# Optimization experiments

Measured on AMD Instinct MI355X. Metric: run time of the kernel, lower is better.

Reference implementation:

```python
import jax, jax.numpy as jnp
import numpy as np

B, T, DIM, H, DH = 4, 2048, 1024, 16, 64
NEG = -1.0e9


def setup_inputs() -> dict:
    key = jax.random.key(0)
    ks = jax.random.split(key, 12)
    inner = H * DH
    s_in = 1.0 / np.sqrt(DIM)
    s_out = 1.0 / np.sqrt(inner)
    q = jax.random.normal(ks[0], (B, T, DIM), jnp.float32)
    k = jax.random.normal(ks[1], (B, T, DIM), jnp.float32)
    v = jax.random.normal(ks[2], (B, T, DIM), jnp.float32)
    # nn.Linear weights stored as [out, in]; we keep [in, out] for x @ W
    W_q = jax.random.uniform(ks[3], (DIM, inner), jnp.float32, -s_in, s_in)
    b_q = jax.random.uniform(ks[4], (inner,), jnp.float32, -s_in, s_in)
    W_k = jax.random.uniform(ks[5], (DIM, inner), jnp.float32, -s_in, s_in)
    b_k = jax.random.uniform(ks[6], (inner,), jnp.float32, -s_in, s_in)
    W_v = jax.random.uniform(ks[7], (DIM, inner), jnp.float32, -s_in, s_in)
    b_v = jax.random.uniform(ks[8], (inner,), jnp.float32, -s_in, s_in)
    W_o = jax.random.uniform(ks[9], (inner, DIM), jnp.float32, -s_out, s_out)
    b_o = jax.random.uniform(ks[10], (DIM,), jnp.float32, -s_out, s_out)
    # causal mask: True = masked (strict upper triangle), broadcastable [1,1,T,T]
    causal_mask = jnp.triu(jnp.ones((T, T), bool), k=1)[None, None]
    # context mask: True = keep; random padding pattern with col 0 always valid
    context_mask = jax.random.bernoulli(ks[11], 0.9, (B, T)).at[:, 0].set(True)
    return {"q": q, "k": k, "v": v,
            "W_q": W_q, "b_q": b_q, "W_k": W_k, "b_k": b_k,
            "W_v": W_v, "b_v": b_v, "W_o": W_o, "b_o": b_o,
            "causal_mask": causal_mask, "context_mask": context_mask}


def reference(q, k, v, W_q, b_q, W_k, b_k, W_v, b_v, W_o, b_o,
              causal_mask, context_mask):
    scale = DH ** -0.5
    split = lambda x: x.reshape(x.shape[0], x.shape[1], H, DH).transpose(0, 2, 1, 3)
    qh = split(q @ W_q + b_q)  # [b,h,t,d]
    kh = split(k @ W_k + b_k)
    vh = split(v @ W_v + b_v)
    scores = jnp.einsum('bhid,bhjd->bhij', qh * scale, kh)
    scores = jnp.where(context_mask[:, None, None, :], scores, NEG)
    scores = jnp.where(causal_mask, NEG, scores)
    probs = jax.nn.softmax(scores, axis=-1)
    out = jnp.einsum('bhij,bhjd->bhid', probs, vh)
    out = out.transpose(0, 2, 1, 3).reshape(B, T, H * DH)
    return out @ W_o + b_o
```

## Files before the change

kernel.cpp:

```cpp
#include <hip/hip_runtime.h>
#include <hip/hip_bf16.h>
#include <cstdint>
#include <cstddef>

#define DEV static __device__ __forceinline__

typedef __attribute__((ext_vector_type(8))) short short8;
typedef __attribute__((ext_vector_type(4))) float floatx4;

#define BB 4
#define TT 2048
#define DIMM 1024
#define HH 16
#define DHH 64
#define MM (BB*TT)
#define QBLK 128
#define NQT (TT/QBLK)
#define M0F 12.0f

DEV unsigned short f2bu(float f) {
    unsigned int u = __float_as_uint(f);
    unsigned int r = (u + 0x7fffu + ((u >> 16) & 1u)) >> 16;
    return (unsigned short)r;
}

DEV unsigned long long pack4(float a, float b, float c, float d) {
    return (unsigned long long)f2bu(a) | ((unsigned long long)f2bu(b) << 16) |
           ((unsigned long long)f2bu(c) << 32) | ((unsigned long long)f2bu(d) << 48);
}

DEV unsigned int pk2(float lo, float hi) {
    __hip_bfloat162 h = __float22bfloat162_rn(make_float2(lo, hi));
    unsigned int r;
    __builtin_memcpy(&r, &h, 4);
    return r;
}

DEV unsigned long long pk4(float a, float b, float c, float d) {
    return (unsigned long long)pk2(a, b) | ((unsigned long long)pk2(c, d) << 32);
}

DEV void gload16(const void* g, void* l) {
    __builtin_amdgcn_global_load_lds(
        (const __attribute__((address_space(1))) unsigned int*)g,
        (__attribute__((address_space(3))) unsigned int*)l, 16, 0, 0);
}

#define MFMA16(a, b, c) __builtin_amdgcn_mfma_f32_16x16x32_bf16((a), (b), (c), 0, 0, 0)

__global__ __launch_bounds__(256) void ctx_bias(const unsigned char* __restrict__ raw,
                                                float* __restrict__ out) {
    __shared__ int nz1, nz23;
    if (threadIdx.x == 0) { nz1 = 0; nz23 = 0; }
    __syncthreads();
    int a1 = 0, a23 = 0;
    for (int i = threadIdx.x; i < BB * TT; i += 256) {
        unsigned char vb = raw[i];
        int m = i & 3;
        if (vb) { if (m == 1) a1 = 1; else if (m >= 2) a23 = 1; }
    }
    if (a1) atomicOr(&nz1, 1);
    if (a23) atomicOr(&nz23, 1);
    __syncthreads();
    const int mode = nz1 ? 2 : (nz23 ? 1 : 0);
    for (int i = threadIdx.x; i < BB * TT; i += 256) {
        bool keep;
        if (mode == 2)      keep = raw[i] != 0;
        else if (mode == 0) keep = raw[(size_t)4 * i] != 0;
        else                keep = (raw[(size_t)4 * i + 2] | raw[(size_t)4 * i + 3]) != 0;
        out[i] = keep ? -M0F : -3.0e38f;
    }
}

__global__ __launch_bounds__(256) void wtrans(const float* __restrict__ W0, const float* __restrict__ W1,
                                              const float* __restrict__ W2, const float* __restrict__ W3,
                                              unsigned short* __restrict__ out) {
    const float* W = blockIdx.y == 0 ? W0 : blockIdx.y == 1 ? W1 : blockIdx.y == 2 ? W2 : W3;
    unsigned short* O = out + (size_t)blockIdx.y * DIMM * DIMM;
    const int tx = blockIdx.x & 15, ty = blockIdx.x >> 4;
    __shared__ float s[64][65];
    const int tid = threadIdx.x;
#pragma unroll
    for (int j = 0; j < 4; ++j) {
        int c = tid + 256 * j;
        int r = c >> 4, c4 = c & 15;
        float4 vv = *reinterpret_cast<const float4*>(&W[(size_t)(ty * 64 + r) * DIMM + tx * 64 + c4 * 4]);
        s[r][c4 * 4 + 0] = vv.x; s[r][c4 * 4 + 1] = vv.y;
        s[r][c4 * 4 + 2] = vv.z; s[r][c4 * 4 + 3] = vv.w;
    }
    __syncthreads();
#pragma unroll
    for (int j = 0; j < 4; ++j) {
        int c = tid + 256 * j;
        int n = c >> 4, k4 = c & 15;
        unsigned long long pk = pack4(s[k4 * 4 + 0][n], s[k4 * 4 + 1][n], s[k4 * 4 + 2][n], s[k4 * 4 + 3][n]);
        *reinterpret_cast<unsigned long long*>(&O[(size_t)(tx * 64 + n) * DIMM + ty * 64 + k4 * 4]) = pk;
    }
}

__global__ __launch_bounds__(256) void proj3(const float* __restrict__ qin, const float* __restrict__ kin,
                                             const float* __restrict__ vin, const unsigned short* __restrict__ Wt,
                                             const float* __restrict__ bq, const float* __restrict__ bk,
                                             const float* __restrict__ bv,
                                             unsigned short* __restrict__ Qp, unsigned short* __restrict__ Kp,
                                             unsigned short* __restrict__ Vtp, float scale_q) {
    const int z = blockIdx.z;
    const float* Af = z == 0 ? qin : z == 1 ? kin : vin;
    const unsigned short* Bt = Wt + (size_t)z * DIMM * DIMM;
    const float* bias = z == 0 ? bq : z == 1 ? bk : bv;
    const float scale = z == 0 ? scale_q : 1.f;

    __shared__ unsigned short As[128 * 32];
    __shared__ unsigned short Bs[128 * 32];
    const int tid = threadIdx.x, lane = tid & 63, g = lane >> 4, lq = lane & 15;
    const int wid = tid >> 6;
    const int mbase = blockIdx.x * 128, nbase = blockIdx.y * 128;
    const int wm = (wid >> 1) * 64, wn = (wid & 1) * 64;
    floatx4 acc[4][4];
#pragma unroll
    for (int i = 0; i < 4; ++i)
#pragma unroll
        for (int j = 0; j < 4; ++j) acc[i][j] = (floatx4){0.f, 0.f, 0.f, 0.f};

    for (int k0 = 0; k0 < DIMM; k0 += 32) {
#pragma unroll
        for (int j = 0; j < 2; ++j) {
            int c = j * 256 + tid;
            int row = c >> 2, kc = c & 3;
            gload16(&Bt[(size_t)(nbase + row) * DIMM + k0 + kc * 8], &Bs[c * 8]);
        }
#pragma unroll
        for (int j = 0; j < 4; ++j) {
            int c = tid + 256 * j;
            int row = c >> 3, kc = c & 7;
            float4 v = *reinterpret_cast<const float4*>(&Af[(size_t)(mbase + row) * DIMM + k0 + kc * 4]);
            *reinterpret_cast<unsigned long long*>(&As[row * 32 + kc * 4]) = pk4(v.x, v.y, v.z, v.w);
        }
        __syncthreads();
        short8 af[4], bfr[4];
#pragma unroll
        for (int i = 0; i < 4; ++i) {
            af[i]  = *reinterpret_cast<const short8*>(&As[(wm + i * 16 + lq) * 32 + g * 8]);
            bfr[i] = *reinterpret_cast<const short8*>(&Bs[(wn + i * 16 + lq) * 32 + g * 8]);
        }
#pragma unroll
        for (int i = 0; i < 4; ++i)
#pragma unroll
            for (int j = 0; j < 4; ++j)
                acc[i][j] = MFMA16(af[i], bfr[j], acc[i][j]);
        __syncthreads();
    }

#pragma unroll
    for (int i = 0; i < 4; ++i) {
#pragma unroll
        for (int j = 0; j < 4; ++j) {
            const int col = nbase + wn + j * 16 + lq;
            const float bvv = bias[col];
            const int row0 = mbase + wm + i * 16 + g * 4;
            if (z < 2) {
                unsigned short* C = z == 0 ? Qp : Kp;
#pragma unroll
                for (int r = 0; r < 4; ++r)
                    C[(size_t)(row0 + r) * DIMM + col] = f2bu((acc[i][j][r] + bvv) * scale);
            } else {
                const int b = row0 >> 11, t0 = row0 & (TT - 1);
                const int h = col >> 6, d = col & 63;
                unsigned long long pk = pk4(acc[i][j][0] + bvv, acc[i][j][1] + bvv,
                                            acc[i][j][2] + bvv, acc[i][j][3] + bvv);
                *reinterpret_cast<unsigned long long*>(
                    &Vtp[((size_t)(b * HH + h) * DHH + d) * TT + t0]) = pk;
            }
        }
    }
}

__global__ __launch_bounds__(256) void gemm_out(const unsigned short* __restrict__ Ab,
                                                const unsigned short* __restrict__ Bt,
                                                const float* __restrict__ bias,
                                                float* __restrict__ C) {
    __shared__ unsigned short As[128 * 32];
    __shared__ unsigned short Bs[128 * 32];
    const int tid = threadIdx.x, lane = tid & 63, g = lane >> 4, lq = lane & 15;
    const int wid = tid >> 6;
    const int mbase = blockIdx.x * 128, nbase = blockIdx.y * 128;
    const int wm = (wid >> 1) * 64, wn = (wid & 1) * 64;
    floatx4 acc[4][4];
#pragma unroll
    for (int i = 0; i < 4; ++i)
#pragma unroll
        for (int j = 0; j < 4; ++j) acc[i][j] = (floatx4){0.f, 0.f, 0.f, 0.f};

    for (int k0 = 0; k0 < DIMM; k0 += 32) {
#pragma unroll
        for (int j = 0; j < 2; ++j) {
            int c = j * 256 + tid;
            int row = c >> 2, kc = c & 3;
            gload16(&Bt[(size_t)(nbase + row) * DIMM + k0 + kc * 8], &Bs[c * 8]);
            gload16(&Ab[(size_t)(mbase + row) * DIMM + k0 + kc * 8], &As[c * 8]);
        }
        __syncthreads();
        short8 af[4], bfr[4];
#pragma unroll
        for (int i = 0; i < 4; ++i) {
            af[i]  = *reinterpret_cast<const short8*>(&As[(wm + i * 16 + lq) * 32 + g * 8]);
            bfr[i] = *reinterpret_cast<const short8*>(&Bs[(wn + i * 16 + lq) * 32 + g * 8]);
        }
#pragma unroll
        for (int i = 0; i < 4; ++i)
#pragma unroll
            for (int j = 0; j < 4; ++j)
                acc[i][j] = MFMA16(af[i], bfr[j], acc[i][j]);
        __syncthreads();
    }

#pragma unroll
    for (int i = 0; i < 4; ++i) {
#pragma unroll
        for (int j = 0; j < 4; ++j) {
            const int col = nbase + wn + j * 16 + lq;
            const float bv = bias[col];
            const int row0 = mbase + wm + i * 16 + g * 4;
#pragma unroll
            for (int r = 0; r < 4; ++r)
                C[(size_t)(row0 + r) * DIMM + col] = acc[i][j][r] + bv;
        }
    }
}

__global__ __launch_bounds__(512, 4) void attn128(const unsigned short* __restrict__ Q,
                                                  const unsigned short* __restrict__ Km,
                                                  const unsigned short* __restrict__ Vt,
                                                  const float* __restrict__ ctxb,
                                                  unsigned short* __restrict__ O) {
    const int pair = blockIdx.x & 7, h = (blockIdx.x >> 3) & 15, b = blockIdx.x >> 7;
    const int tid = threadIdx.x, lane = tid & 63, g = lane >> 4, lq = lane & 15, wid = tid >> 6;

    __shared__ unsigned short Qs[QBLK * 64];
    __shared__ unsigned short Ks[2][64 * 64];
    __shared__ unsigned short Vs[2][64 * 64];
    __shared__ unsigned short Ps[8][16 * 72];

    const float* cbias = ctxb + b * TT;
    const unsigned short* Vbase = Vt + (size_t)(b * HH + h) * DHH * TT;
    const int srow = tid >> 3, sdc = tid & 7;
    const int soff = (srow * 128 + sdc * 16) ^ ((srow & 7) << 4);

    for (int part = 0; part < 2; ++part) {
        const int qt = (part == 0) ? pair : (NQT - 1 - pair);
        const int qbase = qt * QBLK;
        const size_t rowQ = (size_t)(b * TT + qbase);
        const int nkv = 2 * qt + 2;

        __syncthreads();
#pragma unroll
        for (int j = 0; j < 2; ++j) {
            int ci = j * 512 + tid;
            int row = ci >> 3, dc = ci & 7;
            *reinterpret_cast<float4*>((char*)Qs + ((row * 128 + dc * 16) ^ ((row & 7) << 4))) =
                *reinterpret_cast<const float4*>(&Q[(rowQ + row) * DIMM + h * DHH + dc * 8]);
        }
        {
            float4 k0v = *reinterpret_cast<const float4*>(&Km[(size_t)(b * TT + srow) * DIMM + h * DHH + sdc * 8]);
            float4 v0v = *reinterpret_cast<const float4*>(&Vbase[(size_t)srow * TT + sdc * 8]);
            *reinterpret_cast<float4*>((char*)Ks[0] + soff) = k0v;
            *reinterpret_cast<float4*>((char*)Vs[0] + soff) = v0v;
        }
        __syncthreads();

        short8 qf0, qf1;
        {
            const int r = wid * 16 + lq;
            const int sw = (r & 7) << 4;
            qf0 = *reinterpret_cast<const short8*>((char*)Qs + ((r * 128 + g * 16) ^ sw));
            qf1 = *reinterpret_cast<const short8*>((char*)Qs + ((r * 128 + 64 + g * 16) ^ sw));
        }

        floatx4 oacc[4];
#pragma unroll
        for (int f = 0; f < 4; ++f) oacc[f] = (floatx4){0.f, 0.f, 0.f, 0.f};
        float l_run = 0.f;
        const int qwave_min = qbase + wid * 16;
        const int qg = qwave_min + lq;

        for (int kt = 0; kt < nkv; ++kt) {
            const int cur = kt & 1;
            const int kvb = kt * 64;
            const bool pf = (kt + 1 < nkv);
            float4 kreg, vreg;
            if (pf) {
                const int kvn = kvb + 64;
                kreg = *reinterpret_cast<const float4*>(&Km[(size_t)(b * TT + kvn + srow) * DIMM + h * DHH + sdc * 8]);
                vreg = *reinterpret_cast<const float4*>(&Vbase[(size_t)srow * TT + kvn + sdc * 8]);
            }
            if (kvb <= qwave_min + 15) {
                const bool needC = (kvb + 63 > qwave_min);
                float p[4][4];
                __builtin_amdgcn_s_setprio(1);
#pragma unroll
                for (int f = 0; f < 4; ++f) {
                    const int r = f * 16 + lq;
                    const int sw = (r & 7) << 4;
                    short8 kf0 = *reinterpret_cast<const short8*>((char*)Ks[cur] + ((r * 128 + g * 16) ^ sw));
                    short8 kf1 = *reinterpret_cast<const short8*>((char*)Ks[cur] + ((r * 128 + 64 + g * 16) ^ sw));
                    const float4 bias = *reinterpret_cast<const float4*>(&cbias[kvb + f * 16 + g * 4]);
                    floatx4 t = (floatx4){bias.x, bias.y, bias.z, bias.w};
                    t = MFMA16(kf0, qf0, t);
                    t = MFMA16(kf1, qf1, t);
#pragma unroll
                    for (int r2 = 0; r2 < 4; ++r2) {
                        float sv = t[r2];
                        if (needC) {
                            const int kv = kvb + f * 16 + g * 4 + r2;
                            if (kv > qg) sv = -3.0e38f;
                        }
                        p[f][r2] = exp2f(sv);
                    }
                }
                __builtin_amdgcn_s_setprio(0);
                float rs = 0.f;
#pragma unroll
                for (int f = 0; f < 4; ++f)
#pragma unroll
                    for (int r2 = 0; r2 < 4; ++r2) rs += p[f][r2];
                rs += __shfl_xor(rs, 16, 64);
                rs += __shfl_xor(rs, 32, 64);
                l_run += rs;
#pragma unroll
                for (int f = 0; f < 4; ++f)
                    *reinterpret_cast<unsigned long long*>(&Ps[wid][lq * 72 + f * 16 + g * 4]) =
                        pk4(p[f][0], p[f][1], p[f][2], p[f][3]);
                __builtin_amdgcn_s_setprio(1);
#pragma unroll
                for (int f = 0; f < 4; ++f) {
                    const int r = f * 16 + lq;
                    const int sw = (r & 7) << 4;
#pragma unroll
                    for (int kk = 0; kk < 2; ++kk) {
                        short8 av = *reinterpret_cast<const short8*>((char*)Vs[cur] + ((r * 128 + kk * 64 + g * 16) ^ sw));
                        short8 bv = *reinterpret_cast<const short8*>(&Ps[wid][lq * 72 + kk * 32 + g * 8]);
                        oacc[f] = MFMA16(av, bv, oacc[f]);
                    }
                }
                __builtin_amdgcn_s_setprio(0);
            }
            if (pf) {
                *reinterpret_cast<float4*>((char*)Ks[cur ^ 1] + soff) = kreg;
                *reinterpret_cast<float4*>((char*)Vs[cur ^ 1] + soff) = vreg;
            }
            __syncthreads();
        }

        const float inv = 1.f / l_run;
#pragma unroll
        for (int f = 0; f < 4; ++f) {
            unsigned long long pk = pk4(oacc[f][0] * inv, oacc[f][1] * inv,
                                        oacc[f][2] * inv, oacc[f][3] * inv);
            *reinterpret_cast<unsigned long long*>(
                &O[(rowQ + wid * 16 + lq) * DIMM + h * DHH + f * 16 + g * 4]) = pk;
        }
    }
}

extern "C" void kernel_launch(void* const* d_in, const int* in_sizes, int n_in,
                              void* d_out, int out_size, void* d_ws, size_t ws_size,
                              hipStream_t stream) {
    const float* q  = (const float*)d_in[0];
    const float* k  = (const float*)d_in[1];
    const float* v  = (const float*)d_in[2];
    const float* Wq = (const float*)d_in[3];
    const float* bq = (const float*)d_in[4];
    const float* Wk = (const float*)d_in[5];
    const float* bk = (const float*)d_in[6];
    const float* Wv = (const float*)d_in[7];
    const float* bv = (const float*)d_in[8];
    const float* Wo = (const float*)d_in[9];
    const float* bo = (const float*)d_in[10];
    const unsigned char* cmask = (const unsigned char*)d_in[12];

    unsigned short* Qp  = (unsigned short*)d_ws;
    unsigned short* Kp  = Qp + (size_t)MM * DIMM;
    unsigned short* Vtp = Kp + (size_t)MM * DIMM;
    unsigned short* AO  = Vtp + (size_t)MM * DIMM;
    unsigned short* Wt  = AO + (size_t)MM * DIMM;
    float* ctxb = (float*)(Wt + (size_t)4 * DIMM * DIMM);

    ctx_bias<<<dim3(1), dim3(256), 0, stream>>>(cmask, ctxb);
    wtrans<<<dim3(256, 4), dim3(256), 0, stream>>>(Wq, Wk, Wv, Wo, Wt);

    const float scale_q = 0.125f * 1.4426950408889634f;
    proj3<<<dim3(64, 8, 3), dim3(256), 0, stream>>>(q, k, v, Wt, bq, bk, bv, Qp, Kp, Vtp, scale_q);

    attn128<<<dim3(BB * HH * 8), dim3(512), 0, stream>>>(Qp, Kp, Vtp, ctxb, AO);

    gemm_out<<<dim3(64, 8), dim3(256), 0, stream>>>(AO, Wt + (size_t)3 * DIMM * DIMM, bo, (float*)d_out);
}
```

Baseline: 248.4 us.

## Pre-convert inputs to bf16 and use unified swizzled K64 GEMM

The fused fp32-input QKV projection kernel is replaced by separate fp32-to-bf16 conversion passes followed by a templated bf16 GEMM. The GEMM uses a 64-wide K tile with XOR-swizzled LDS layout and async global-to-LDS loads for both operands, and the output projection shares the same kernel. The aim is to avoid repeated fp32 loads and in-loop conversion of activation tiles across N blocks, and to cut LDS bank conflicts. The cost is an extra round trip through global memory for the converted inputs and six launches instead of one, with the three projections serialized through a shared scratch buffer.

```diff
diff --git a/kernel.cpp b/kernel.cpp
--- a/kernel.cpp
+++ b/kernel.cpp
@@ -98,20 +98,24 @@
     }
 }
 
-__global__ __launch_bounds__(256) void proj3(const float* __restrict__ qin, const float* __restrict__ kin,
-                                             const float* __restrict__ vin, const unsigned short* __restrict__ Wt,
-                                             const float* __restrict__ bq, const float* __restrict__ bk,
-                                             const float* __restrict__ bv,
-                                             unsigned short* __restrict__ Qp, unsigned short* __restrict__ Kp,
-                                             unsigned short* __restrict__ Vtp, float scale_q) {
-    const int z = blockIdx.z;
-    const float* Af = z == 0 ? qin : z == 1 ? kin : vin;
-    const unsigned short* Bt = Wt + (size_t)z * DIMM * DIMM;
-    const float* bias = z == 0 ? bq : z == 1 ? bk : bv;
-    const float scale = z == 0 ? scale_q : 1.f;
-
-    __shared__ unsigned short As[128 * 32];
-    __shared__ unsigned short Bs[128 * 32];
+__global__ __launch_bounds__(256) void cvt_bf16(const float* __restrict__ in,
+                                                unsigned short* __restrict__ out) {
+    const size_t i = ((size_t)blockIdx.x * 256 + threadIdx.x) * 8;
+    float4 a = *reinterpret_cast<const float4*>(&in[i]);
+    float4 b = *reinterpret_cast<const float4*>(&in[i + 4]);
+    unsigned long long lo = pk4(a.x, a.y, a.z, a.w);
+    unsigned long long hi = pk4(b.x, b.y, b.z, b.w);
+    ulonglong2 v; v.x = lo; v.y = hi;
+    *reinterpret_cast<ulonglong2*>(&out[i]) = v;
+}
+
+template <int OMODE>
+__global__ __launch_bounds__(256) void gemm_bf16(const unsigned short* __restrict__ Ab,
+                                                 const unsigned short* __restrict__ Bt,
+                                                 const float* __restrict__ bias,
+                                                 void* __restrict__ Cp, float scale) {
+    __shared__ unsigned short As[128 * 64];
+    __shared__ unsigned short Bs[128 * 64];
     const int tid = threadIdx.x, lane = tid & 63, g = lane >> 4, lq = lane & 15;
     const int wid = tid >> 6;
     const int mbase = blockIdx.x * 128, nbase = blockIdx.y * 128;
@@ -122,32 +126,32 @@
 #pragma unroll
         for (int j = 0; j < 4; ++j) acc[i][j] = (floatx4){0.f, 0.f, 0.f, 0.f};
 
-    for (int k0 = 0; k0 < DIMM; k0 += 32) {
-#pragma unroll
-        for (int j = 0; j < 2; ++j) {
-            int c = j * 256 + tid;
-            int row = c >> 2, kc = c & 3;
-            gload16(&Bt[(size_t)(nbase + row) * DIMM + k0 + kc * 8], &Bs[c * 8]);
-        }
+    for (int k0 = 0; k0 < DIMM; k0 += 64) {
 #pragma unroll
         for (int j = 0; j < 4; ++j) {
-            int c = tid + 256 * j;
-            int row = c >> 3, kc = c & 7;
-            float4 v = *reinterpret_cast<const float4*>(&Af[(size_t)(mbase + row) * DIMM + k0 + kc * 4]);
-            *reinterpret_cast<unsigned long long*>(&As[row * 32 + kc * 4]) = pk4(v.x, v.y, v.z, v.w);
+            const int c = j * 256 + tid;
+            const int row = c >> 3, ci = c & 7;
+            const int sc = ci ^ (row & 7);
+            gload16(&Ab[(size_t)(mbase + row) * DIMM + k0 + sc * 8], &As[c * 8]);
+            gload16(&Bt[(size_t)(nbase + row) * DIMM + k0 + sc * 8], &Bs[c * 8]);
         }
         __syncthreads();
-        short8 af[4], bfr[4];
-#pragma unroll
-        for (int i = 0; i < 4; ++i) {
-            af[i]  = *reinterpret_cast<const short8*>(&As[(wm + i * 16 + lq) * 32 + g * 8]);
-            bfr[i] = *reinterpret_cast<const short8*>(&Bs[(wn + i * 16 + lq) * 32 + g * 8]);
-        }
-#pragma unroll
-        for (int i = 0; i < 4; ++i)
-#pragma unroll
-            for (int j = 0; j < 4; ++j)
-                acc[i][j] = MFMA16(af[i], bfr[j], acc[i][j]);
+#pragma unroll
+        for (int kk = 0; kk < 2; ++kk) {
+            short8 af[4], bf[4];
+#pragma unroll
+            for (int i = 0; i < 4; ++i) {
+                const int ra = wm + i * 16 + lq;
+                af[i] = *reinterpret_cast<const short8*>(&As[ra * 64 + ((kk * 4 + g) ^ (ra & 7)) * 8]);
+                const int rb = wn + i * 16 + lq;
+                bf[i] = *reinterpret_cast<const short8*>(&Bs[rb * 64 + ((kk * 4 + g) ^ (rb & 7)) * 8]);
+            }
+#pragma unroll
+            for (int i = 0; i < 4; ++i)
+#pragma unroll
+                for (int j2 = 0; j2 < 4; ++j2)
+                    acc[i][j2] = MFMA16(af[i], bf[j2], acc[i][j2]);
+        }
         __syncthreads();
     }
 
@@ -158,72 +162,25 @@
             const int col = nbase + wn + j * 16 + lq;
             const float bvv = bias[col];
             const int row0 = mbase + wm + i * 16 + g * 4;
-            if (z < 2) {
-                unsigned short* C = z == 0 ? Qp : Kp;
+            if (OMODE == 2) {
+                float* C = (float*)Cp;
+#pragma unroll
+                for (int r = 0; r < 4; ++r)
+                    C[(size_t)(row0 + r) * DIMM + col] = acc[i][j][r] + bvv;
+            } else if (OMODE == 0) {
+                unsigned short* C = (unsigned short*)Cp;
 #pragma unroll
                 for (int r = 0; r < 4; ++r)
                     C[(size_t)(row0 + r) * DIMM + col] = f2bu((acc[i][j][r] + bvv) * scale);
             } else {
+                unsigned short* C = (unsigned short*)Cp;
                 const int b = row0 >> 11, t0 = row0 & (TT - 1);
                 const int h = col >> 6, d = col & 63;
                 unsigned long long pk = pk4(acc[i][j][0] + bvv, acc[i][j][1] + bvv,
                                             acc[i][j][2] + bvv, acc[i][j][3] + bvv);
                 *reinterpret_cast<unsigned long long*>(
-                    &Vtp[((size_t)(b * HH + h) * DHH + d) * TT + t0]) = pk;
-            }
-        }
-    }
-}
-
-__global__ __launch_bounds__(256) void gemm_out(const unsigned short* __restrict__ Ab,
-                                                const unsigned short* __restrict__ Bt,
-                                                const float* __restrict__ bias,
-                                                float* __restrict__ C) {
-    __shared__ unsigned short As[128 * 32];
-    __shared__ unsigned short Bs[128 * 32];
-    const int tid = threadIdx.x, lane = tid & 63, g = lane >> 4, lq = lane & 15;
-    const int wid = tid >> 6;
-    const int mbase = blockIdx.x * 128, nbase = blockIdx.y * 128;
-    const int wm = (wid >> 1) * 64, wn = (wid & 1) * 64;
-    floatx4 acc[4][4];
-#pragma unroll
-    for (int i = 0; i < 4; ++i)
-#pragma unroll
-        for (int j = 0; j < 4; ++j) acc[i][j] = (floatx4){0.f, 0.f, 0.f, 0.f};
-
-    for (int k0 = 0; k0 < DIMM; k0 += 32) {
-#pragma unroll
-        for (int j = 0; j < 2; ++j) {
-            int c = j * 256 + tid;
-            int row = c >> 2, kc = c & 3;
-            gload16(&Bt[(size_t)(nbase + row) * DIMM + k0 + kc * 8], &Bs[c * 8]);
-            gload16(&Ab[(size_t)(mbase + row) * DIMM + k0 + kc * 8], &As[c * 8]);
-        }
-        __syncthreads();
-        short8 af[4], bfr[4];
-#pragma unroll
-        for (int i = 0; i < 4; ++i) {
-            af[i]  = *reinterpret_cast<const short8*>(&As[(wm + i * 16 + lq) * 32 + g * 8]);
-            bfr[i] = *reinterpret_cast<const short8*>(&Bs[(wn + i * 16 + lq) * 32 + g * 8]);
-        }
-#pragma unroll
-        for (int i = 0; i < 4; ++i)
-#pragma unroll
-            for (int j = 0; j < 4; ++j)
-                acc[i][j] = MFMA16(af[i], bfr[j], acc[i][j]);
-        __syncthreads();
-    }
-
-#pragma unroll
-    for (int i = 0; i < 4; ++i) {
-#pragma unroll
-        for (int j = 0; j < 4; ++j) {
-            const int col = nbase + wn + j * 16 + lq;
-            const float bv = bias[col];
-            const int row0 = mbase + wm + i * 16 + g * 4;
-#pragma unroll
-            for (int r = 0; r < 4; ++r)
-                C[(size_t)(row0 + r) * DIMM + col] = acc[i][j][r] + bv;
+                    &C[((size_t)(b * HH + h) * DHH + d) * TT + t0]) = pk;
+            }
         }
     }
 }
@@ -389,9 +346,15 @@
     wtrans<<<dim3(256, 4), dim3(256), 0, stream>>>(Wq, Wk, Wv, Wo, Wt);
 
     const float scale_q = 0.125f * 1.4426950408889634f;
-    proj3<<<dim3(64, 8, 3), dim3(256), 0, stream>>>(q, k, v, Wt, bq, bk, bv, Qp, Kp, Vtp, scale_q);
+
+    cvt_bf16<<<dim3(4096), dim3(256), 0, stream>>>(q, AO);
+    gemm_bf16<0><<<dim3(64, 8), dim3(256), 0, stream>>>(AO, Wt,                           bq, Qp,  scale_q);
+    cvt_bf16<<<dim3(4096), dim3(256), 0, stream>>>(k, AO);
+    gemm_bf16<0><<<dim3(64, 8), dim3(256), 0, stream>>>(AO, Wt + (size_t)DIMM * DIMM,     bk, Kp,  1.f);
+    cvt_bf16<<<dim3(4096), dim3(256), 0, stream>>>(v, AO);
+    gemm_bf16<1><<<dim3(64, 8), dim3(256), 0, stream>>>(AO, Wt + (size_t)2 * DIMM * DIMM, bv, Vtp, 1.f);
 
     attn128<<<dim3(BB * HH * 8), dim3(512), 0, stream>>>(Qp, Kp, Vtp, ctxb, AO);
 
-    gemm_out<<<dim3(64, 8), dim3(256), 0, stream>>>(AO, Wt + (size_t)3 * DIMM * DIMM, bo, (float*)d_out);
-}
+    gemm_bf16<2><<<dim3(64, 8), dim3(256), 0, stream>>>(AO, Wt + (size_t)3 * DIMM * DIMM, bo, d_out, 1.f);
+}
```

After: 234.7 us. 1.06x faster.
